# Kernel tuning notes

Hardware: AMD Instinct MI355X
Metric: run time of the kernel (lower is better)

The kernel has to match this reference:

```python
import jax, jax.numpy as jnp
import numpy as np

N = 100000   # nodes
D = 64       # in_features
E = 1200000  # edges (avg degree ~12)
C = 1.0      # curvature
MIN_NORM = 1e-15
PROJ_EPS = 4e-3  # float32 eps used by HGCN-style PoincareBall.proj


def setup_inputs() -> dict:
    key = jax.random.key(0)
    k1, k2, k3 = jax.random.split(key, 3)
    x = jax.random.normal(k1, (N, D), dtype=jnp.float32) * 0.1
    edge_index = jax.random.randint(k2, (2, E), 0, N, dtype=jnp.int32)
    # GCNConv learned params (lin weight + bias)
    W = jax.random.normal(k3, (D, D), dtype=jnp.float32) / np.sqrt(D)
    b = jnp.zeros((D,), dtype=jnp.float32)
    return {"x": x, "W": W, "b": b, "edge_index": edge_index}


def expmap0(u, c):
    sqrt_c = jnp.sqrt(c)
    u_norm = jnp.maximum(jnp.linalg.norm(u, axis=-1, keepdims=True), MIN_NORM)
    return jnp.tanh(sqrt_c * u_norm) * u / (sqrt_c * u_norm)


def proj(x, c):
    norm = jnp.maximum(jnp.linalg.norm(x, axis=-1, keepdims=True), MIN_NORM)
    maxnorm = (1.0 - PROJ_EPS) / jnp.sqrt(c)
    return jnp.where(norm > maxnorm, x / norm * maxnorm, x)


def gcn_conv(x, W, b, edge_index, n_nodes):
    # PyG GCNConv: h = x @ W; add self-loops; symmetric normalization; scatter-add; + bias
    h = x @ W  # [N, D]
    src, dst = edge_index[0], edge_index[1]
    loops = jnp.arange(n_nodes, dtype=edge_index.dtype)
    s = jnp.concatenate([src, loops])  # [E+N]
    d = jnp.concatenate([dst, loops])
    deg = jax.ops.segment_sum(jnp.ones(s.shape, dtype=h.dtype), d, num_segments=n_nodes)
    deg_inv_sqrt = jnp.where(deg > 0, deg ** -0.5, 0.0)
    norm = deg_inv_sqrt[s] * deg_inv_sqrt[d]  # [E+N]
    msgs = h[s] * norm[:, None]               # gather + scale: [E+N, D]
    out = jax.ops.segment_sum(msgs, d, num_segments=n_nodes)  # scatter-add
    return out + b


def reference(x, W, b, edge_index):
    # Note: original computes logmap0(x) but discards it (conv uses raw x) -- dead code.
    support_t = gcn_conv(x, W, b, edge_index, N)
    return proj(expmap0(support_t, C), C)
```

## Files before the change

kernel.cpp:

```cpp
#include <hip/hip_runtime.h>
#include <hip/hip_bf16.h>

#define DFEAT 64
#define NBSH  8
#define NPB   256
#define EPB   8192

__global__ __launch_bounds__(256) void histA_kernel(const int* __restrict__ ei,
                                                    int* __restrict__ blkhist, int E) {
    __shared__ int h[512];
    int t = threadIdx.x;
    h[t] = 0; h[t + 256] = 0;
    __syncthreads();
    int base = blockIdx.x * EPB;
    #pragma unroll
    for (int i = 0; i < EPB / 256; ++i) {
        int e = base + i * 256 + t;
        if (e < E) atomicAdd(&h[ei[E + e] >> NBSH], 1);
    }
    __syncthreads();
    blkhist[blockIdx.x * 512 + t]       = h[t];
    blkhist[blockIdx.x * 512 + t + 256] = h[t + 256];
}

__global__ __launch_bounds__(512) void scanB_kernel(int* __restrict__ blkhist,
                                                    int* __restrict__ bucketbase, int nblk) {
    __shared__ int lds[512];
    int t = threadIdx.x;
    int run = 0;
    for (int blk = 0; blk < nblk; ++blk) {
        int idx = blk * 512 + t;
        int v = blkhist[idx];
        blkhist[idx] = run;
        run += v;
    }
    lds[t] = run;
    __syncthreads();
    int s = run;
    for (int off = 1; off < 512; off <<= 1) {
        int y = (t >= off) ? lds[t - off] : 0;
        __syncthreads();
        lds[t] += y;
        __syncthreads();
    }
    bucketbase[t] = lds[t] - s;
}

__global__ __launch_bounds__(256) void partC_kernel(const int* __restrict__ ei,
                                                    const int* __restrict__ blkhist,
                                                    const int* __restrict__ bucketbase,
                                                    unsigned* __restrict__ ebuf, int E) {
    __shared__ int cur[512];
    int t = threadIdx.x;
    cur[t]       = bucketbase[t]       + blkhist[blockIdx.x * 512 + t];
    cur[t + 256] = bucketbase[t + 256] + blkhist[blockIdx.x * 512 + t + 256];
    __syncthreads();
    int base = blockIdx.x * EPB;
    #pragma unroll
    for (int i = 0; i < EPB / 256; ++i) {
        int e = base + i * 256 + t;
        if (e < E) {
            int s = ei[e];
            int d = ei[E + e];
            int pos = atomicAdd(&cur[d >> NBSH], 1);
            ebuf[pos] = (unsigned)s | ((unsigned)(d & (NPB - 1)) << 17);
        }
    }
}

__global__ __launch_bounds__(256) void csrD_kernel(const unsigned* __restrict__ ebuf,
                                                   const int* __restrict__ bucketbase,
                                                   int* __restrict__ srcs,
                                                   int* __restrict__ begs,
                                                   int* __restrict__ lens,
                                                   float* __restrict__ dinv, int n) {
    __shared__ int cnt[256];
    __shared__ int tmp[256];
    int t = threadIdx.x;
    int b = blockIdx.x;
    int ebeg = bucketbase[b], eend = bucketbase[b + 1];
    int regionbase = ebeg + b * (4 * NPB);
    cnt[t] = 0;
    __syncthreads();
    for (int e = ebeg + t; e < eend; e += 256)
        atomicAdd(&cnt[ebuf[e] >> 17], 1);
    __syncthreads();
    int nid = (b << NBSH) + t;
    int deg = cnt[t];
    int slots = (nid < n) ? ((deg + 4) & ~3) : 0;
    tmp[t] = slots;
    __syncthreads();
    int s = slots;
    for (int o = 1; o < 256; o <<= 1) {
        int y = (t >= o) ? tmp[t - o] : 0;
        __syncthreads();
        tmp[t] += y;
        __syncthreads();
    }
    int excl = tmp[t] - s;
    if (nid < n) {
        int beg_abs = regionbase + excl;
        begs[nid] = beg_abs;
        lens[nid] = slots;
        dinv[nid] = rsqrtf((float)(deg + 1));
        srcs[beg_abs] = nid;
        for (int k = deg + 1; k < slots; ++k) srcs[beg_abs + k] = n;
    }
    cnt[t] = excl + 1;
    __syncthreads();
    for (int e = ebeg + t; e < eend; e += 256) {
        unsigned v = ebuf[e];
        int pos = atomicAdd(&cnt[v >> 17], 1);
        srcs[regionbase + pos] = (int)(v & 0x1ffffu);
    }
}

__global__ __launch_bounds__(256) void xsprep_kernel(const float* __restrict__ x,
                                                     const float* __restrict__ dinv,
                                                     unsigned* __restrict__ xs, int n) {
    int i = blockIdx.x * blockDim.x + threadIdx.x;
    int total = (n + 1) * 32;
    if (i >= total) return;
    int row = i >> 5, col = i & 31;
    unsigned v = 0;
    if (row < n) {
        float di = dinv[row];
        float f0 = x[row * DFEAT + 2 * col] * di;
        float f1 = x[row * DFEAT + 2 * col + 1] * di;
        unsigned u0 = __float_as_uint(f0); u0 = (u0 + 0x7fffu + ((u0 >> 16) & 1u)) >> 16;
        unsigned u1 = __float_as_uint(f1); u1 = (u1 + 0x7fffu + ((u1 >> 16) & 1u)) >> 16;
        v = (u0 & 0xffffu) | (u1 << 16);
    }
    xs[i] = v;
}

__global__ __launch_bounds__(256) void agg_kernel(const int* __restrict__ begs,
                                                  const int* __restrict__ lens,
                                                  const int* __restrict__ srcs,
                                                  const float* __restrict__ dinv,
                                                  const uint2* __restrict__ xs2,
                                                  const float* __restrict__ W,
                                                  const float* __restrict__ b,
                                                  float* __restrict__ out,
                                                  int n, int nquads) {
    __shared__ float Wl[DFEAT * DFEAT];
    __shared__ float xl[4][DFEAT];
    int t = threadIdx.x;
    #pragma unroll
    for (int i = 0; i < 16; ++i) Wl[i * 256 + t] = W[i * 256 + t];
    __syncthreads();

    int r = t >> 6, lane = t & 63;
    int g = lane >> 4;
    int q = lane & 15;
    float bias = b[lane];

    for (int quad = blockIdx.x; quad < nquads; quad += gridDim.x) {
        int node = quad * 4 + r;
        if (node >= n) continue;

        float f0 = 0, f1 = 0, f2 = 0, f3 = 0;
        int beg = begs[node];
        int end = beg + lens[node];
        for (int base = beg; base < end; base += 64) {
            int m = end - base; if (m > 64) m = 64;
            int idx = 0;
            if (lane < m) idx = srcs[base + lane];
            int quads_ = m >> 2;
            for (int j = 0; j < quads_; ++j) {
                int sv = __shfl(idx, 4 * j + g, 64);
                uint2 d = xs2[(unsigned)sv * 16 + q];
                f0 += __uint_as_float(d.x << 16);
                f1 += __uint_as_float(d.x & 0xffff0000u);
                f2 += __uint_as_float(d.y << 16);
                f3 += __uint_as_float(d.y & 0xffff0000u);
            }
        }
        #pragma unroll
        for (int off = 16; off < 64; off <<= 1) {
            f0 += __shfl_xor(f0, off, 64);
            f1 += __shfl_xor(f1, off, 64);
            f2 += __shfl_xor(f2, off, 64);
            f3 += __shfl_xor(f3, off, 64);
        }
        if (g == 0) {
            float di = dinv[node];
            xl[r][4 * q + 0] = f0 * di;
            xl[r][4 * q + 1] = f1 * di;
            xl[r][4 * q + 2] = f2 * di;
            xl[r][4 * q + 3] = f3 * di;
        }

        float o0 = bias, o1 = 0.0f;
        #pragma unroll
        for (int k = 0; k < DFEAT; k += 2) {
            o0 = fmaf(xl[r][k],     Wl[k * DFEAT + lane],       o0);
            o1 = fmaf(xl[r][k + 1], Wl[(k + 1) * DFEAT + lane], o1);
        }
        float o = o0 + o1;

        float ss = o * o;
        #pragma unroll
        for (int off = 32; off > 0; off >>= 1) ss += __shfl_xor(ss, off, 64);
        float norm = fmaxf(sqrtf(ss), 1e-15f);
        float tn = tanhf(norm);
        float scale = fminf(tn, 1.0f - 4e-3f) / norm;
        out[(long long)node * DFEAT + lane] = o * scale;
    }
}


extern "C" void kernel_launch(void* const* d_in, const int* in_sizes, int n_in,
                              void* d_out, int out_size, void* d_ws, size_t ws_size,
                              hipStream_t stream) {
    const float* x = (const float*)d_in[0];
    const float* W = (const float*)d_in[1];
    const float* b = (const float*)d_in[2];
    const int* ei  = (const int*)d_in[3];

    int n = in_sizes[0] / DFEAT;
    int E = in_sizes[3] / 2;
    int NB = (n + NPB - 1) / NPB;
    int nblk = (E + EPB - 1) / EPB;
    int nquads = (n + 3) / 4;

    int* blkhist    = (int*)d_ws;
    int* bucketbase = blkhist + nblk * 512;
    int* srcs       = bucketbase + 512;
    int* begs       = srcs + E + NB * 4 * NPB;
    int* lens       = begs + n;
    float* dinv     = (float*)(lens + n);
    unsigned* ebuf  = (unsigned*)(dinv + n);
    unsigned* xs    = ebuf;

    float* out = (float*)d_out;

    int aggblocks = 2048;
    if (aggblocks > nquads) aggblocks = nquads;

    histA_kernel <<<nblk, 256, 0, stream>>>(ei, blkhist, E);
    scanB_kernel <<<1, 512, 0, stream>>>(blkhist, bucketbase, nblk);
    partC_kernel <<<nblk, 256, 0, stream>>>(ei, blkhist, bucketbase, ebuf, E);
    csrD_kernel  <<<NB, 256, 0, stream>>>(ebuf, bucketbase, srcs, begs, lens, dinv, n);
    xsprep_kernel<<<((n + 1) * 32 + 255) / 256, 256, 0, stream>>>(x, dinv, xs, n);
    agg_kernel   <<<aggblocks, 256, 0, stream>>>(begs, lens, srcs, dinv,
                                                 (const uint2*)xs, W, b, out, n, nquads);
}
```

Before: 225.6 us.

## Parallelize bucket scan across blocks and aggregate two nodes per wavefront

Transposes the per-block bucket histogram so the serial single-block scan can become a 512-block segmented scan followed by a small scan of the bucket totals. This removes a long sequential loop over edge blocks that ran in one workgroup. The aggregation kernel now has each wavefront process two nodes at once with interleaved gathers, which raises memory-level parallelism and reuses each W load for two nodes. The cost is an extra kernel launch, higher register pressure, and divergence when the two nodes have different degrees. The scan assumes nblk is at most 256 (147 for this input).

```diff
diff --git a/kernel.cpp b/kernel.cpp
--- a/kernel.cpp
+++ b/kernel.cpp
@@ -7,7 +7,8 @@
 #define EPB   8192
 
 __global__ __launch_bounds__(256) void histA_kernel(const int* __restrict__ ei,
-                                                    int* __restrict__ blkhist, int E) {
+                                                    int* __restrict__ blkhistT,
+                                                    int E, int nblk) {
     __shared__ int h[512];
     int t = threadIdx.x;
     h[t] = 0; h[t + 256] = 0;
@@ -19,24 +20,37 @@
         if (e < E) atomicAdd(&h[ei[E + e] >> NBSH], 1);
     }
     __syncthreads();
-    blkhist[blockIdx.x * 512 + t]       = h[t];
-    blkhist[blockIdx.x * 512 + t + 256] = h[t + 256];
-}
-
-__global__ __launch_bounds__(512) void scanB_kernel(int* __restrict__ blkhist,
-                                                    int* __restrict__ bucketbase, int nblk) {
+    blkhistT[t * nblk + blockIdx.x]         = h[t];
+    blkhistT[(t + 256) * nblk + blockIdx.x] = h[t + 256];
+}
+
+__global__ __launch_bounds__(256) void scanB1_kernel(int* __restrict__ blkhistT,
+                                                     int* __restrict__ buckettotal, int nblk) {
+    __shared__ int lds[256];
+    int t = threadIdx.x;
+    int b = blockIdx.x;
+    int v = (t < nblk) ? blkhistT[b * nblk + t] : 0;
+    lds[t] = v;
+    __syncthreads();
+    #pragma unroll
+    for (int off = 1; off < 256; off <<= 1) {
+        int y = (t >= off) ? lds[t - off] : 0;
+        __syncthreads();
+        lds[t] += y;
+        __syncthreads();
+    }
+    if (t < nblk) blkhistT[b * nblk + t] = lds[t] - v;
+    if (t == 255) buckettotal[b] = lds[255];
+}
+
+__global__ __launch_bounds__(512) void scanB2_kernel(const int* __restrict__ buckettotal,
+                                                     int* __restrict__ bucketbase) {
     __shared__ int lds[512];
     int t = threadIdx.x;
-    int run = 0;
-    for (int blk = 0; blk < nblk; ++blk) {
-        int idx = blk * 512 + t;
-        int v = blkhist[idx];
-        blkhist[idx] = run;
-        run += v;
-    }
-    lds[t] = run;
-    __syncthreads();
-    int s = run;
+    int s = buckettotal[t];
+    lds[t] = s;
+    __syncthreads();
+    #pragma unroll
     for (int off = 1; off < 512; off <<= 1) {
         int y = (t >= off) ? lds[t - off] : 0;
         __syncthreads();
@@ -44,16 +58,17 @@
         __syncthreads();
     }
     bucketbase[t] = lds[t] - s;
+    if (t == 511) bucketbase[512] = lds[511];
 }
 
 __global__ __launch_bounds__(256) void partC_kernel(const int* __restrict__ ei,
-                                                    const int* __restrict__ blkhist,
+                                                    const int* __restrict__ blkhistT,
                                                     const int* __restrict__ bucketbase,
-                                                    unsigned* __restrict__ ebuf, int E) {
+                                                    unsigned* __restrict__ ebuf, int E, int nblk) {
     __shared__ int cur[512];
     int t = threadIdx.x;
-    cur[t]       = bucketbase[t]       + blkhist[blockIdx.x * 512 + t];
-    cur[t + 256] = bucketbase[t + 256] + blkhist[blockIdx.x * 512 + t + 256];
+    cur[t]       = bucketbase[t]       + blkhistT[t * nblk + blockIdx.x];
+    cur[t + 256] = bucketbase[t + 256] + blkhistT[(t + 256) * nblk + blockIdx.x];
     __syncthreads();
     int base = blockIdx.x * EPB;
     #pragma unroll
@@ -142,9 +157,9 @@
                                                   const float* __restrict__ W,
                                                   const float* __restrict__ b,
                                                   float* __restrict__ out,
-                                                  int n, int nquads) {
+                                                  int n, int noctets) {
     __shared__ float Wl[DFEAT * DFEAT];
-    __shared__ float xl[4][DFEAT];
+    __shared__ float xl[8][DFEAT];
     int t = threadIdx.x;
     #pragma unroll
     for (int i = 0; i < 16; ++i) Wl[i * 256 + t] = W[i * 256 + t];
@@ -155,57 +170,112 @@
     int q = lane & 15;
     float bias = b[lane];
 
-    for (int quad = blockIdx.x; quad < nquads; quad += gridDim.x) {
-        int node = quad * 4 + r;
-        if (node >= n) continue;
-
-        float f0 = 0, f1 = 0, f2 = 0, f3 = 0;
-        int beg = begs[node];
-        int end = beg + lens[node];
-        for (int base = beg; base < end; base += 64) {
-            int m = end - base; if (m > 64) m = 64;
-            int idx = 0;
-            if (lane < m) idx = srcs[base + lane];
-            int quads_ = m >> 2;
-            for (int j = 0; j < quads_; ++j) {
-                int sv = __shfl(idx, 4 * j + g, 64);
-                uint2 d = xs2[(unsigned)sv * 16 + q];
-                f0 += __uint_as_float(d.x << 16);
-                f1 += __uint_as_float(d.x & 0xffff0000u);
-                f2 += __uint_as_float(d.y << 16);
-                f3 += __uint_as_float(d.y & 0xffff0000u);
+    for (int oct = blockIdx.x; oct < noctets; oct += gridDim.x) {
+        int na = oct * 8 + r;
+        int nb_ = na + 4;
+        bool va = na < n, vb = nb_ < n;
+        if (!va) continue;
+
+        int beg0 = begs[na],  end0 = beg0 + lens[na];
+        int beg1 = 0, end1 = 0;
+        if (vb) { beg1 = begs[nb_]; end1 = beg1 + lens[nb_]; }
+
+        float a0 = 0, a1 = 0, a2 = 0, a3 = 0;
+        float b0 = 0, b1 = 0, b2 = 0, b3 = 0;
+        int base0 = beg0, base1 = beg1;
+        while (base0 < end0 || base1 < end1) {
+            int m0 = end0 - base0; m0 = m0 < 0 ? 0 : (m0 > 64 ? 64 : m0);
+            int m1 = end1 - base1; m1 = m1 < 0 ? 0 : (m1 > 64 ? 64 : m1);
+            int idx0 = 0, idx1 = 0;
+            if (lane < m0) idx0 = srcs[base0 + lane];
+            if (lane < m1) idx1 = srcs[base1 + lane];
+            int q0 = m0 >> 2, q1 = m1 >> 2;
+            int qc = q0 < q1 ? q0 : q1;
+            for (int j = 0; j < qc; ++j) {
+                int sv0 = __shfl(idx0, 4 * j + g, 64);
+                int sv1 = __shfl(idx1, 4 * j + g, 64);
+                uint2 d0 = xs2[(unsigned)sv0 * 16 + q];
+                uint2 d1 = xs2[(unsigned)sv1 * 16 + q];
+                a0 += __uint_as_float(d0.x << 16);
+                a1 += __uint_as_float(d0.x & 0xffff0000u);
+                a2 += __uint_as_float(d0.y << 16);
+                a3 += __uint_as_float(d0.y & 0xffff0000u);
+                b0 += __uint_as_float(d1.x << 16);
+                b1 += __uint_as_float(d1.x & 0xffff0000u);
+                b2 += __uint_as_float(d1.y << 16);
+                b3 += __uint_as_float(d1.y & 0xffff0000u);
             }
+            for (int j = qc; j < q0; ++j) {
+                int sv0 = __shfl(idx0, 4 * j + g, 64);
+                uint2 d0 = xs2[(unsigned)sv0 * 16 + q];
+                a0 += __uint_as_float(d0.x << 16);
+                a1 += __uint_as_float(d0.x & 0xffff0000u);
+                a2 += __uint_as_float(d0.y << 16);
+                a3 += __uint_as_float(d0.y & 0xffff0000u);
+            }
+            for (int j = qc; j < q1; ++j) {
+                int sv1 = __shfl(idx1, 4 * j + g, 64);
+                uint2 d1 = xs2[(unsigned)sv1 * 16 + q];
+                b0 += __uint_as_float(d1.x << 16);
+                b1 += __uint_as_float(d1.x & 0xffff0000u);
+                b2 += __uint_as_float(d1.y << 16);
+                b3 += __uint_as_float(d1.y & 0xffff0000u);
+            }
+            base0 += 64; base1 += 64;
         }
         #pragma unroll
         for (int off = 16; off < 64; off <<= 1) {
-            f0 += __shfl_xor(f0, off, 64);
-            f1 += __shfl_xor(f1, off, 64);
-            f2 += __shfl_xor(f2, off, 64);
-            f3 += __shfl_xor(f3, off, 64);
+            a0 += __shfl_xor(a0, off, 64);
+            a1 += __shfl_xor(a1, off, 64);
+            a2 += __shfl_xor(a2, off, 64);
+            a3 += __shfl_xor(a3, off, 64);
+            b0 += __shfl_xor(b0, off, 64);
+            b1 += __shfl_xor(b1, off, 64);
+            b2 += __shfl_xor(b2, off, 64);
+            b3 += __shfl_xor(b3, off, 64);
         }
         if (g == 0) {
-            float di = dinv[node];
-            xl[r][4 * q + 0] = f0 * di;
-            xl[r][4 * q + 1] = f1 * di;
-            xl[r][4 * q + 2] = f2 * di;
-            xl[r][4 * q + 3] = f3 * di;
-        }
-
-        float o0 = bias, o1 = 0.0f;
+            float dia = dinv[na];
+            xl[r][4 * q + 0] = a0 * dia;
+            xl[r][4 * q + 1] = a1 * dia;
+            xl[r][4 * q + 2] = a2 * dia;
+            xl[r][4 * q + 3] = a3 * dia;
+            if (vb) {
+                float dib = dinv[nb_];
+                xl[r + 4][4 * q + 0] = b0 * dib;
+                xl[r + 4][4 * q + 1] = b1 * dib;
+                xl[r + 4][4 * q + 2] = b2 * dib;
+                xl[r + 4][4 * q + 3] = b3 * dib;
+            }
+        }
+
+        float oa0 = bias, oa1 = 0.0f, ob0 = bias, ob1 = 0.0f;
         #pragma unroll
         for (int k = 0; k < DFEAT; k += 2) {
-            o0 = fmaf(xl[r][k],     Wl[k * DFEAT + lane],       o0);
-            o1 = fmaf(xl[r][k + 1], Wl[(k + 1) * DFEAT + lane], o1);
-        }
-        float o = o0 + o1;
-
-        float ss = o * o;
+            float w0 = Wl[k * DFEAT + lane];
+            float w1 = Wl[(k + 1) * DFEAT + lane];
+            oa0 = fmaf(xl[r][k],     w0, oa0);
+            oa1 = fmaf(xl[r][k + 1], w1, oa1);
+            ob0 = fmaf(xl[r + 4][k],     w0, ob0);
+            ob1 = fmaf(xl[r + 4][k + 1], w1, ob1);
+        }
+        float oa = oa0 + oa1;
+        float ob = ob0 + ob1;
+
+        float ssa = oa * oa, ssb = ob * ob;
         #pragma unroll
-        for (int off = 32; off > 0; off >>= 1) ss += __shfl_xor(ss, off, 64);
-        float norm = fmaxf(sqrtf(ss), 1e-15f);
-        float tn = tanhf(norm);
-        float scale = fminf(tn, 1.0f - 4e-3f) / norm;
-        out[(long long)node * DFEAT + lane] = o * scale;
+        for (int off = 32; off > 0; off >>= 1) {
+            ssa += __shfl_xor(ssa, off, 64);
+            ssb += __shfl_xor(ssb, off, 64);
+        }
+        float norma = fmaxf(sqrtf(ssa), 1e-15f);
+        float sca = fminf(tanhf(norma), 1.0f - 4e-3f) / norma;
+        out[(long long)na * DFEAT + lane] = oa * sca;
+        if (vb) {
+            float normb = fmaxf(sqrtf(ssb), 1e-15f);
+            float scb = fminf(tanhf(normb), 1.0f - 4e-3f) / normb;
+            out[(long long)nb_ * DFEAT + lane] = ob * scb;
+        }
     }
 }
 
@@ -222,27 +292,29 @@
     int E = in_sizes[3] / 2;
     int NB = (n + NPB - 1) / NPB;
     int nblk = (E + EPB - 1) / EPB;
-    int nquads = (n + 3) / 4;
-
-    int* blkhist    = (int*)d_ws;
-    int* bucketbase = blkhist + nblk * 512;
-    int* srcs       = bucketbase + 512;
-    int* begs       = srcs + E + NB * 4 * NPB;
-    int* lens       = begs + n;
-    float* dinv     = (float*)(lens + n);
-    unsigned* ebuf  = (unsigned*)(dinv + n);
-    unsigned* xs    = ebuf;
+    int noctets = (n + 7) / 8;
+
+    int* blkhistT    = (int*)d_ws;
+    int* buckettotal = blkhistT + 512 * nblk;
+    int* bucketbase  = buckettotal + 512;
+    int* srcs        = bucketbase + 516;
+    int* begs        = srcs + E + NB * 4 * NPB;
+    int* lens        = begs + n;
+    float* dinv      = (float*)(lens + n);
+    unsigned* ebuf   = (unsigned*)(dinv + n);
+    unsigned* xs     = ebuf;
 
     float* out = (float*)d_out;
 
     int aggblocks = 2048;
-    if (aggblocks > nquads) aggblocks = nquads;
-
-    histA_kernel <<<nblk, 256, 0, stream>>>(ei, blkhist, E);
-    scanB_kernel <<<1, 512, 0, stream>>>(blkhist, bucketbase, nblk);
-    partC_kernel <<<nblk, 256, 0, stream>>>(ei, blkhist, bucketbase, ebuf, E);
+    if (aggblocks > noctets) aggblocks = noctets;
+
+    histA_kernel <<<nblk, 256, 0, stream>>>(ei, blkhistT, E, nblk);
+    scanB1_kernel<<<512, 256, 0, stream>>>(blkhistT, buckettotal, nblk);
+    scanB2_kernel<<<1, 512, 0, stream>>>(buckettotal, bucketbase);
+    partC_kernel <<<nblk, 256, 0, stream>>>(ei, blkhistT, bucketbase, ebuf, E, nblk);
     csrD_kernel  <<<NB, 256, 0, stream>>>(ebuf, bucketbase, srcs, begs, lens, dinv, n);
     xsprep_kernel<<<((n + 1) * 32 + 255) / 256, 256, 0, stream>>>(x, dinv, xs, n);
     agg_kernel   <<<aggblocks, 256, 0, stream>>>(begs, lens, srcs, dinv,
-                                                 (const uint2*)xs, W, b, out, n, nquads);
-}
+                                                 (const uint2*)xs, W, b, out, n, noctets);
+}
```

New measurement: 195.4 us. 1.15x faster.
